# Kernel optimization log

Hardware: AMD Instinct MI355X
Metric: run time of the kernel (lower is better)

The kernel has to match this reference:

```python
import jax, jax.numpy as jnp
import numpy as np

E = 16          # num_experts
H = 2048        # hidden_size
I = 768         # moe_intermediate_size
T = 2048        # tokens (batch*seq)
K = 2           # top_k


def setup_inputs() -> dict:
    key = jax.random.key(0)
    k1, k2, k3, k4, k5 = jax.random.split(key, 5)
    hidden_states = jax.random.normal(k1, (T, H), dtype=jnp.float32)
    top_k_index = jax.random.randint(k2, (T, K), 0, E, dtype=jnp.int32)
    w = jax.random.uniform(k3, (T, K), dtype=jnp.float32)
    top_k_weights = w / jnp.sum(w, axis=-1, keepdims=True)  # softmax-like router weights
    init_std = 0.02
    gate_up_proj = jax.random.normal(k4, (E, 2 * I, H), dtype=jnp.float32) * init_std
    down_proj = jax.random.normal(k5, (E, H, I), dtype=jnp.float32) * init_std
    return {
        "hidden_states": hidden_states,
        "top_k_index": top_k_index,
        "top_k_weights": top_k_weights,
        "gate_up_proj": gate_up_proj,
        "down_proj": down_proj,
    }


def reference(hidden_states, top_k_index, top_k_weights, gate_up_proj, down_proj):
    # Combine matrix C[t, e] = sum_k top_k_weights[t, k] * 1[top_k_index[t,k] == e]
    # Tokens not routed to expert e get weight 0, so the dense-masked compute
    # below is mathematically identical to the per-expert gather/scatter loop.
    t_idx = jnp.arange(T)[:, None]
    C = jnp.zeros((T, E), dtype=hidden_states.dtype).at[t_idx, top_k_index].add(top_k_weights)

    # gate/up projection for every (token, expert): [T, E, 2I]
    gu = jnp.einsum('th,egh->teg', hidden_states, gate_up_proj)
    gate, up = jnp.split(gu, 2, axis=-1)                  # [T, E, I] each
    mid = jax.nn.silu(gate) * up                          # SwiGLU, [T, E, I]
    # down projection fused with routed combine weights -> [T, H]
    out = jnp.einsum('tei,ehi,te->th', mid, down_proj, C)
    return out
```

## Files before the change

kernel.cpp:

```cpp
#include <hip/hip_runtime.h>

#define T_TOK 2048
#define HID   2048
#define IMID  768
#define NEXP  16
#define TOPK  2

#define NPAIR (T_TOK * TOPK)
#define SLACK 64
#define NSLOT (NPAIR + SLACK)

#define BM 64
#define BK 32
#define LDSS 40

typedef __attribute__((ext_vector_type(8))) short short8;
typedef __attribute__((ext_vector_type(4))) float floatx4;

__device__ __forceinline__ short f2bf(float f) {
    union { float f; unsigned u; } v; v.f = f;
    unsigned r = (v.u + 0x7FFFu + ((v.u >> 16) & 1u)) >> 16;
    return (short)r;
}

__device__ __forceinline__ void load_cvt8(const float* __restrict__ p, short* dst) {
    float4 x = *(const float4*)p;
    float4 y = *(const float4*)(p + 4);
    short8 v;
    v[0] = f2bf(x.x); v[1] = f2bf(x.y); v[2] = f2bf(x.z); v[3] = f2bf(x.w);
    v[4] = f2bf(y.x); v[5] = f2bf(y.y); v[6] = f2bf(y.z); v[7] = f2bf(y.w);
    *(short8*)dst = v;
}

__global__ void k_count(const int* __restrict__ idx, int* __restrict__ counts) {
    int i = blockIdx.x * blockDim.x + threadIdx.x;
    if (i < NPAIR) atomicAdd(&counts[idx[i]], 1);
}

__global__ void k_scan(const int* __restrict__ counts, int* __restrict__ base,
                       int* __restrict__ cursor) {
    int s = 0;
    for (int e = 0; e < NEXP; e++) { base[e] = s; cursor[e] = s; s += counts[e]; }
}

__global__ void k_scatter(const int* __restrict__ idx, const float* __restrict__ w,
                          int* __restrict__ cursor, int* __restrict__ tok,
                          float* __restrict__ wgt) {
    int i = blockIdx.x * blockDim.x + threadIdx.x;
    if (i < NPAIR) {
        int e = idx[i];
        int p = atomicAdd(&cursor[e], 1);
        tok[p] = i / TOPK;
        wgt[p] = w[i];
    }
}

__global__ __launch_bounds__(256) void k_gemm1(
    const float* __restrict__ hs, const float* __restrict__ gup,
    const int* __restrict__ counts, const int* __restrict__ base,
    const int* __restrict__ tok, short* __restrict__ mid)
{
    const int e = blockIdx.z, rt = blockIdx.y, ct = blockIdx.x;
    const int n = counts[e];
    if (rt * BM >= n) return;
    const int rowbase = base[e] + rt * BM;

    __shared__ short sA[BM][LDSS];
    __shared__ short sBg[BM][LDSS];
    __shared__ short sBu[BM][LDSS];
    __shared__ int s_tok[BM];

    const int tid = threadIdx.x;
    if (tid < BM) s_tok[tid] = tok[rowbase + tid];
    __syncthreads();

    const int lrow = tid >> 2;
    const int cg   = (tid & 3) * 8;

    const float* aptr = hs + (size_t)s_tok[lrow] * HID + cg;
    const float* gptr = gup + (size_t)e * (2 * IMID) * HID + (size_t)(ct * 64 + lrow) * HID + cg;
    const float* uptr = gptr + (size_t)IMID * HID;

    const int wave = tid >> 6;
    const int lane = tid & 63;
    const int m16  = lane & 15;
    const int quad = lane >> 4;

    floatx4 accg[4], accu[4];
#pragma unroll
    for (int i = 0; i < 4; i++) { accg[i] = (floatx4)0.0f; accu[i] = (floatx4)0.0f; }

    for (int k0 = 0; k0 < HID; k0 += BK) {
        load_cvt8(aptr + k0, &sA[lrow][cg]);
        load_cvt8(gptr + k0, &sBg[lrow][cg]);
        load_cvt8(uptr + k0, &sBu[lrow][cg]);
        __syncthreads();
        short8 af = *(const short8*)&sA[wave * 16 + m16][quad * 8];
#pragma unroll
        for (int cf = 0; cf < 4; cf++) {
            short8 bg = *(const short8*)&sBg[cf * 16 + m16][quad * 8];
            short8 bu = *(const short8*)&sBu[cf * 16 + m16][quad * 8];
            accg[cf] = __builtin_amdgcn_mfma_f32_16x16x32_bf16(af, bg, accg[cf], 0, 0, 0);
            accu[cf] = __builtin_amdgcn_mfma_f32_16x16x32_bf16(af, bu, accu[cf], 0, 0, 0);
        }
        __syncthreads();
    }

    const int nvalid = n - rt * BM;
#pragma unroll
    for (int cf = 0; cf < 4; cf++) {
#pragma unroll
        for (int r = 0; r < 4; r++) {
            int row = wave * 16 + quad * 4 + r;
            if (row < nvalid) {
                float g = accg[cf][r], u = accu[cf][r];
                float mval = g / (1.0f + __expf(-g)) * u;
                mid[(size_t)(rowbase + row) * IMID + ct * 64 + cf * 16 + m16] = f2bf(mval);
            }
        }
    }
}

__global__ __launch_bounds__(256) void k_gemm2(
    const float* __restrict__ down, const short* __restrict__ mid,
    const int* __restrict__ counts, const int* __restrict__ base,
    const int* __restrict__ tok, const float* __restrict__ wgt,
    float* __restrict__ out)
{
    const int e = blockIdx.z, rt = blockIdx.y, ht = blockIdx.x;
    const int n = counts[e];
    if (rt * BM >= n) return;
    const int rowbase = base[e] + rt * BM;

    __shared__ short sA[BM][LDSS];
    __shared__ short sB[BM][LDSS];
    __shared__ int   s_tok[BM];
    __shared__ float s_w[BM];

    const int tid = threadIdx.x;
    if (tid < BM) { s_tok[tid] = tok[rowbase + tid]; s_w[tid] = wgt[rowbase + tid]; }

    const int lrow = tid >> 2;
    const int cg   = (tid & 3) * 8;

    const short* aptr = mid + (size_t)(rowbase + lrow) * IMID + cg;
    const float* bptr = down + (size_t)e * HID * IMID + (size_t)(ht * 64 + lrow) * IMID + cg;

    const int wave = tid >> 6;
    const int lane = tid & 63;
    const int m16  = lane & 15;
    const int quad = lane >> 4;

    floatx4 acc[4];
#pragma unroll
    for (int i = 0; i < 4; i++) acc[i] = (floatx4)0.0f;

    for (int k0 = 0; k0 < IMID; k0 += BK) {
        *(short8*)&sA[lrow][cg] = *(const short8*)(aptr + k0);
        load_cvt8(bptr + k0, &sB[lrow][cg]);
        __syncthreads();
        short8 af = *(const short8*)&sA[wave * 16 + m16][quad * 8];
#pragma unroll
        for (int cf = 0; cf < 4; cf++) {
            short8 bf_ = *(const short8*)&sB[cf * 16 + m16][quad * 8];
            acc[cf] = __builtin_amdgcn_mfma_f32_16x16x32_bf16(af, bf_, acc[cf], 0, 0, 0);
        }
        __syncthreads();
    }

    const int nvalid = n - rt * BM;
#pragma unroll
    for (int cf = 0; cf < 4; cf++) {
#pragma unroll
        for (int r = 0; r < 4; r++) {
            int row = wave * 16 + quad * 4 + r;
            if (row < nvalid) {
                int t = s_tok[row];
                float w = s_w[row];
                atomicAdd(&out[(size_t)t * HID + ht * 64 + cf * 16 + m16], w * acc[cf][r]);
            }
        }
    }
}

extern "C" void kernel_launch(void* const* d_in, const int* in_sizes, int n_in,
                              void* d_out, int out_size, void* d_ws, size_t ws_size,
                              hipStream_t stream) {
    const float* hs   = (const float*)d_in[0];
    const int*   idx  = (const int*)d_in[1];
    const float* tkw  = (const float*)d_in[2];
    const float* gup  = (const float*)d_in[3];
    const float* down = (const float*)d_in[4];
    float* out = (float*)d_out;

    char* ws = (char*)d_ws;
    int*   counts = (int*)(ws + 0);
    int*   base   = (int*)(ws + 64);
    int*   cursor = (int*)(ws + 128);
    int*   tok    = (int*)(ws + 256);
    float* wgt    = (float*)(ws + 256 + NSLOT * 4);
    short* mid    = (short*)(ws + 33792);

    hipMemsetAsync(ws, 0, 33792, stream);
    hipMemsetAsync(d_out, 0, (size_t)T_TOK * HID * sizeof(float), stream);

    k_count  <<<(NPAIR + 255) / 256, 256, 0, stream>>>(idx, counts);
    k_scan   <<<1, 1, 0, stream>>>(counts, base, cursor);
    k_scatter<<<(NPAIR + 255) / 256, 256, 0, stream>>>(idx, tkw, cursor, tok, wgt);
    k_gemm1  <<<dim3(IMID / 64, NPAIR / BM, NEXP), 256, 0, stream>>>(hs, gup, counts, base, tok, mid);
    k_gemm2  <<<dim3(HID / 64, NPAIR / BM, NEXP), 256, 0, stream>>>(down, mid, counts, base, tok, wgt, out);
}
```

Baseline: 534.5 us.

## Rewrite MoE pipeline with fused preprocessing, larger tiles, and async double-buffered loads

Routing (count, scan, scatter) now runs in one block of a single preprocessing kernel. The other blocks of that kernel pre-convert the hidden states to bf16. Both GEMMs use 128-row tiles with BK=64, a compact tile list instead of a sparse grid, and double-buffered A tiles loaded via global_load_lds with an XOR swizzle. Weight tiles are register-prefetched one step ahead. Router weights are folded into the SwiGLU output, and GEMM2 uses 128-column tiles. The aims are more data reuse, fewer launches and wasted blocks, and overlap of memory with MFMA, at the cost of higher register and LDS pressure.

```diff
diff --git a/kernel.cpp b/kernel.cpp
--- a/kernel.cpp
+++ b/kernel.cpp
@@ -1,183 +1,319 @@
 #include <hip/hip_runtime.h>
 
-#define T_TOK 2048
+#define TTOK  2048
 #define HID   2048
 #define IMID  768
 #define NEXP  16
-#define TOPK  2
-
-#define NPAIR (T_TOK * TOPK)
-#define SLACK 64
-#define NSLOT (NPAIR + SLACK)
-
-#define BM 64
-#define BK 32
-#define LDSS 40
-
-typedef __attribute__((ext_vector_type(8))) short short8;
-typedef __attribute__((ext_vector_type(4))) float floatx4;
+#define NPAIR 4096
+#define NSLOT 4224
+#define BM    128
+#define BK    64
+#define MAXT  48
+#define LDB   72
+#define ABUF  (128 * 64)
+
+typedef __attribute__((ext_vector_type(8))) short  short8;
+typedef __attribute__((ext_vector_type(4))) float  floatx4;
+typedef __attribute__((ext_vector_type(2))) unsigned uint2v;
+
+__device__ __forceinline__ unsigned pk2(float a, float b) {
+    union { float f; unsigned u; } x{a}, y{b};
+    unsigned ra = (x.u + 0x7FFFu + ((x.u >> 16) & 1u)) >> 16;
+    unsigned rb = (y.u + 0x7FFFu + ((y.u >> 16) & 1u)) & 0xFFFF0000u;
+    return ra | rb;
+}
 
 __device__ __forceinline__ short f2bf(float f) {
     union { float f; unsigned u; } v; v.f = f;
-    unsigned r = (v.u + 0x7FFFu + ((v.u >> 16) & 1u)) >> 16;
-    return (short)r;
-}
-
-__device__ __forceinline__ void load_cvt8(const float* __restrict__ p, short* dst) {
-    float4 x = *(const float4*)p;
-    float4 y = *(const float4*)(p + 4);
-    short8 v;
-    v[0] = f2bf(x.x); v[1] = f2bf(x.y); v[2] = f2bf(x.z); v[3] = f2bf(x.w);
-    v[4] = f2bf(y.x); v[5] = f2bf(y.y); v[6] = f2bf(y.z); v[7] = f2bf(y.w);
-    *(short8*)dst = v;
-}
-
-__global__ void k_count(const int* __restrict__ idx, int* __restrict__ counts) {
-    int i = blockIdx.x * blockDim.x + threadIdx.x;
-    if (i < NPAIR) atomicAdd(&counts[idx[i]], 1);
-}
-
-__global__ void k_scan(const int* __restrict__ counts, int* __restrict__ base,
-                       int* __restrict__ cursor) {
-    int s = 0;
-    for (int e = 0; e < NEXP; e++) { base[e] = s; cursor[e] = s; s += counts[e]; }
-}
-
-__global__ void k_scatter(const int* __restrict__ idx, const float* __restrict__ w,
-                          int* __restrict__ cursor, int* __restrict__ tok,
-                          float* __restrict__ wgt) {
-    int i = blockIdx.x * blockDim.x + threadIdx.x;
-    if (i < NPAIR) {
-        int e = idx[i];
-        int p = atomicAdd(&cursor[e], 1);
-        tok[p] = i / TOPK;
-        wgt[p] = w[i];
-    }
-}
-
-__global__ __launch_bounds__(256) void k_gemm1(
-    const float* __restrict__ hs, const float* __restrict__ gup,
-    const int* __restrict__ counts, const int* __restrict__ base,
-    const int* __restrict__ tok, short* __restrict__ mid)
+    return (short)((v.u + 0x7FFFu + ((v.u >> 16) & 1u)) >> 16);
+}
+
+__device__ __forceinline__ short8 cvt8(float4 a, float4 b) {
+    union { unsigned u[4]; short8 s; } r;
+    r.u[0] = pk2(a.x, a.y); r.u[1] = pk2(a.z, a.w);
+    r.u[2] = pk2(b.x, b.y); r.u[3] = pk2(b.z, b.w);
+    return r.s;
+}
+
+__device__ __forceinline__ void async_cp16(const void* g, void* l) {
+    __builtin_amdgcn_global_load_lds(
+        (const __attribute__((address_space(1))) void*)g,
+        (__attribute__((address_space(3))) void*)l, 16, 0, 0);
+}
+
+__global__ __launch_bounds__(256) void k_pre(
+    const float* __restrict__ hs, const int* __restrict__ idx,
+    const float* __restrict__ tkw, int* __restrict__ ntiles,
+    int4* __restrict__ tiles, int* __restrict__ tok,
+    float* __restrict__ wgt, short* __restrict__ X)
 {
-    const int e = blockIdx.z, rt = blockIdx.y, ct = blockIdx.x;
-    const int n = counts[e];
-    if (rt * BM >= n) return;
-    const int rowbase = base[e] + rt * BM;
-
-    __shared__ short sA[BM][LDSS];
-    __shared__ short sBg[BM][LDSS];
-    __shared__ short sBu[BM][LDSS];
-    __shared__ int s_tok[BM];
-
     const int tid = threadIdx.x;
-    if (tid < BM) s_tok[tid] = tok[rowbase + tid];
-    __syncthreads();
-
-    const int lrow = tid >> 2;
-    const int cg   = (tid & 3) * 8;
-
-    const float* aptr = hs + (size_t)s_tok[lrow] * HID + cg;
-    const float* gptr = gup + (size_t)e * (2 * IMID) * HID + (size_t)(ct * 64 + lrow) * HID + cg;
-    const float* uptr = gptr + (size_t)IMID * HID;
-
-    const int wave = tid >> 6;
-    const int lane = tid & 63;
-    const int m16  = lane & 15;
-    const int quad = lane >> 4;
-
-    floatx4 accg[4], accu[4];
-#pragma unroll
-    for (int i = 0; i < 4; i++) { accg[i] = (floatx4)0.0f; accu[i] = (floatx4)0.0f; }
-
-    for (int k0 = 0; k0 < HID; k0 += BK) {
-        load_cvt8(aptr + k0, &sA[lrow][cg]);
-        load_cvt8(gptr + k0, &sBg[lrow][cg]);
-        load_cvt8(uptr + k0, &sBu[lrow][cg]);
-        __syncthreads();
-        short8 af = *(const short8*)&sA[wave * 16 + m16][quad * 8];
-#pragma unroll
-        for (int cf = 0; cf < 4; cf++) {
-            short8 bg = *(const short8*)&sBg[cf * 16 + m16][quad * 8];
-            short8 bu = *(const short8*)&sBu[cf * 16 + m16][quad * 8];
-            accg[cf] = __builtin_amdgcn_mfma_f32_16x16x32_bf16(af, bg, accg[cf], 0, 0, 0);
-            accu[cf] = __builtin_amdgcn_mfma_f32_16x16x32_bf16(af, bu, accu[cf], 0, 0, 0);
-        }
-        __syncthreads();
-    }
-
-    const int nvalid = n - rt * BM;
-#pragma unroll
-    for (int cf = 0; cf < 4; cf++) {
-#pragma unroll
-        for (int r = 0; r < 4; r++) {
-            int row = wave * 16 + quad * 4 + r;
-            if (row < nvalid) {
-                float g = accg[cf][r], u = accu[cf][r];
-                float mval = g / (1.0f + __expf(-g)) * u;
-                mid[(size_t)(rowbase + row) * IMID + ct * 64 + cf * 16 + m16] = f2bf(mval);
-            }
-        }
-    }
-}
-
-__global__ __launch_bounds__(256) void k_gemm2(
-    const float* __restrict__ down, const short* __restrict__ mid,
-    const int* __restrict__ counts, const int* __restrict__ base,
+    if (blockIdx.x == 0) {
+        __shared__ int cnt[NEXP], cur[NEXP];
+        if (tid < NEXP) cnt[tid] = 0;
+        __syncthreads();
+        for (int i = tid; i < NPAIR; i += 256) atomicAdd(&cnt[idx[i]], 1);
+        __syncthreads();
+        if (tid == 0) {
+            int s = 0, nt = 0;
+            for (int e = 0; e < NEXP; e++) {
+                cur[e] = s;
+                int n = cnt[e];
+                for (int tt = 0; tt * BM < n; tt++) {
+                    tiles[nt] = make_int4(e, s + tt * BM, min(BM, n - tt * BM), 0);
+                    nt++;
+                }
+                s += n;
+            }
+            *ntiles = nt;
+        }
+        __syncthreads();
+        for (int i = tid; i < NPAIR; i += 256) {
+            int e = idx[i];
+            int p = atomicAdd(&cur[e], 1);
+            tok[p] = i >> 1;
+            wgt[p] = tkw[i];
+        }
+        for (int i = NPAIR + tid; i < NSLOT; i += 256) { tok[i] = 0; wgt[i] = 0.0f; }
+    } else {
+        const int row = blockIdx.x - 1;
+        const float* src = hs + (size_t)row * HID + tid * 8;
+        float4 a = *(const float4*)src;
+        float4 b = *(const float4*)(src + 4);
+        *(short8*)(X + (size_t)row * HID + tid * 8) = cvt8(a, b);
+    }
+}
+
+__global__ __launch_bounds__(256, 2) void k_gemm1(
+    const float* __restrict__ gup, const short* __restrict__ X,
+    const int* __restrict__ ntiles, const int4* __restrict__ tiles,
     const int* __restrict__ tok, const float* __restrict__ wgt,
-    float* __restrict__ out)
+    short* __restrict__ mid)
 {
-    const int e = blockIdx.z, rt = blockIdx.y, ht = blockIdx.x;
-    const int n = counts[e];
-    if (rt * BM >= n) return;
-    const int rowbase = base[e] + rt * BM;
-
-    __shared__ short sA[BM][LDSS];
-    __shared__ short sB[BM][LDSS];
+    if ((int)blockIdx.y >= *ntiles) return;
+    const int4 td = tiles[blockIdx.y];
+    const int e = td.x, rowstart = td.y, nvalid = td.z;
+    const int ct = blockIdx.x;
+
+    __shared__ short sA[2 * ABUF];
+    __shared__ short sB[128 * LDB];
     __shared__ int   s_tok[BM];
     __shared__ float s_w[BM];
 
     const int tid = threadIdx.x;
-    if (tid < BM) { s_tok[tid] = tok[rowbase + tid]; s_w[tid] = wgt[rowbase + tid]; }
-
-    const int lrow = tid >> 2;
-    const int cg   = (tid & 3) * 8;
-
-    const short* aptr = mid + (size_t)(rowbase + lrow) * IMID + cg;
-    const float* bptr = down + (size_t)e * HID * IMID + (size_t)(ht * 64 + lrow) * IMID + cg;
-
-    const int wave = tid >> 6;
-    const int lane = tid & 63;
-    const int m16  = lane & 15;
-    const int quad = lane >> 4;
-
-    floatx4 acc[4];
-#pragma unroll
-    for (int i = 0; i < 4; i++) acc[i] = (floatx4)0.0f;
-
-    for (int k0 = 0; k0 < IMID; k0 += BK) {
-        *(short8*)&sA[lrow][cg] = *(const short8*)(aptr + k0);
-        load_cvt8(bptr + k0, &sB[lrow][cg]);
-        __syncthreads();
-        short8 af = *(const short8*)&sA[wave * 16 + m16][quad * 8];
-#pragma unroll
-        for (int cf = 0; cf < 4; cf++) {
-            short8 bf_ = *(const short8*)&sB[cf * 16 + m16][quad * 8];
-            acc[cf] = __builtin_amdgcn_mfma_f32_16x16x32_bf16(af, bf_, acc[cf], 0, 0, 0);
-        }
-        __syncthreads();
-    }
-
-    const int nvalid = n - rt * BM;
-#pragma unroll
-    for (int cf = 0; cf < 4; cf++) {
+    if (tid < BM) { s_tok[tid] = tok[rowstart + tid]; s_w[tid] = wgt[rowstart + tid]; }
+    __syncthreads();
+
+    const int wave = tid >> 6, lane = tid & 63;
+    const int m16 = lane & 15, quad = lane >> 4;
+
+    const int lrow = tid >> 3;
+    const int gsw  = (tid & 7) ^ (lrow & 7);
+    const short* aga[4];
+#pragma unroll
+    for (int j = 0; j < 4; j++)
+        aga[j] = X + (size_t)s_tok[lrow + j * 32] * HID + gsw * 8;
+
+    const int colgrp = tid & 15;
+    const int rowoff = tid >> 4;
+    const float* bgate = gup + ((size_t)e * (2 * IMID) + ct * 64) * HID;
+    const float* bup   = bgate + (size_t)IMID * HID;
+
+    float4 br[8];
+    auto loadB = [&](int k0) {
+#pragma unroll
+        for (int i = 0; i < 8; i++) {
+            int brow = i * 16 + rowoff;
+            const float* p = (i < 4) ? (bgate + (size_t)brow * HID)
+                                     : (bup + (size_t)(brow - 64) * HID);
+            br[i] = *(const float4*)(p + k0 + colgrp * 4);
+        }
+    };
+    auto issueA = [&](int k0, short* dst) {
+#pragma unroll
+        for (int j = 0; j < 4; j++)
+            async_cp16(aga[j] + k0, dst + j * 2048 + wave * 512);
+    };
+
+    const int Wm = (wave >> 1) << 6;
+    const int Wi = (wave & 1) << 5;
+    floatx4 ag[4][2], au[4][2];
+#pragma unroll
+    for (int a = 0; a < 4; a++)
+#pragma unroll
+        for (int b = 0; b < 2; b++) { ag[a][b] = (floatx4)0.0f; au[a][b] = (floatx4)0.0f; }
+
+    loadB(0);
+    issueA(0, sA);
+
+    const int nsteps = HID / BK;
+    for (int ks = 0; ks < nsteps; ks++) {
+        short* Acur  = sA + (ks & 1) * ABUF;
+        short* Anext = sA + ((ks + 1) & 1) * ABUF;
+
+#pragma unroll
+        for (int i = 0; i < 8; i++) {
+            int brow = i * 16 + rowoff;
+            uint2v w2;
+            w2.x = pk2(br[i].x, br[i].y);
+            w2.y = pk2(br[i].z, br[i].w);
+            *(uint2v*)&sB[brow * LDB + colgrp * 4] = w2;
+        }
+        __syncthreads();
+
+        if (ks + 1 < nsteps) {
+            issueA((ks + 1) * BK, Anext);
+            loadB((ks + 1) * BK);
+        }
+
+#pragma unroll
+        for (int h = 0; h < 2; h++) {
+            short8 af[4];
+#pragma unroll
+            for (int mf = 0; mf < 4; mf++) {
+                int row = Wm + mf * 16 + m16;
+                int gc = (h * 4 + quad) ^ (row & 7);
+                af[mf] = *(const short8*)&Acur[row * 64 + gc * 8];
+            }
+#pragma unroll
+            for (int nf = 0; nf < 2; nf++) {
+                const short8 bg = *(const short8*)&sB[(Wi + nf * 16 + m16) * LDB + h * 32 + quad * 8];
+                const short8 bu = *(const short8*)&sB[(64 + Wi + nf * 16 + m16) * LDB + h * 32 + quad * 8];
+#pragma unroll
+                for (int mf = 0; mf < 4; mf++) {
+                    ag[mf][nf] = __builtin_amdgcn_mfma_f32_16x16x32_bf16(af[mf], bg, ag[mf][nf], 0, 0, 0);
+                    au[mf][nf] = __builtin_amdgcn_mfma_f32_16x16x32_bf16(af[mf], bu, au[mf][nf], 0, 0, 0);
+                }
+            }
+        }
+        __syncthreads();
+    }
+
+#pragma unroll
+    for (int mf = 0; mf < 4; mf++) {
 #pragma unroll
         for (int r = 0; r < 4; r++) {
-            int row = wave * 16 + quad * 4 + r;
-            if (row < nvalid) {
-                int t = s_tok[row];
-                float w = s_w[row];
-                atomicAdd(&out[(size_t)t * HID + ht * 64 + cf * 16 + m16], w * acc[cf][r]);
+            int m = Wm + mf * 16 + quad * 4 + r;
+            if (m < nvalid) {
+                float w = s_w[m];
+                size_t rowp = (size_t)(rowstart + m) * IMID + ct * 64;
+#pragma unroll
+                for (int nf = 0; nf < 2; nf++) {
+                    float g = ag[mf][nf][r], u = au[mf][nf][r];
+                    float val = g / (1.0f + __expf(-g)) * u * w;
+                    mid[rowp + Wi + nf * 16 + m16] = f2bf(val);
+                }
+            }
+        }
+    }
+}
+
+__global__ __launch_bounds__(256, 2) void k_gemm2(
+    const float* __restrict__ down, const short* __restrict__ mid,
+    const int* __restrict__ ntiles, const int4* __restrict__ tiles,
+    const int* __restrict__ tok, float* __restrict__ out)
+{
+    if ((int)blockIdx.y >= *ntiles) return;
+    const int4 td = tiles[blockIdx.y];
+    const int e = td.x, rowstart = td.y, nvalid = td.z;
+    const int ct = blockIdx.x;
+
+    __shared__ short sA[2 * ABUF];
+    __shared__ short sB[128 * LDB];
+    __shared__ int   s_tok[BM];
+
+    const int tid = threadIdx.x;
+    if (tid < BM) s_tok[tid] = tok[rowstart + tid];
+    __syncthreads();
+
+    const int wave = tid >> 6, lane = tid & 63;
+    const int m16 = lane & 15, quad = lane >> 4;
+
+    const int lrow = tid >> 3;
+    const int gsw  = (tid & 7) ^ (lrow & 7);
+    const short* aga[4];
+#pragma unroll
+    for (int j = 0; j < 4; j++)
+        aga[j] = mid + (size_t)(rowstart + lrow + j * 32) * IMID + gsw * 8;
+
+    const int colgrp = tid & 15;
+    const int rowoff = tid >> 4;
+    const float* bbase = down + ((size_t)e * HID + ct * 128) * IMID;
+
+    float4 br[8];
+    auto loadB = [&](int k0) {
+#pragma unroll
+        for (int i = 0; i < 8; i++)
+            br[i] = *(const float4*)(bbase + (size_t)(i * 16 + rowoff) * IMID + k0 + colgrp * 4);
+    };
+    auto issueA = [&](int k0, short* dst) {
+#pragma unroll
+        for (int j = 0; j < 4; j++)
+            async_cp16(aga[j] + k0, dst + j * 2048 + wave * 512);
+    };
+
+    const int Wm = (wave >> 1) << 6;
+    const int Wn = (wave & 1) << 6;
+    floatx4 acc[4][4];
+#pragma unroll
+    for (int a = 0; a < 4; a++)
+#pragma unroll
+        for (int b = 0; b < 4; b++) acc[a][b] = (floatx4)0.0f;
+
+    loadB(0);
+    issueA(0, sA);
+
+    const int nsteps = IMID / BK;
+    for (int ks = 0; ks < nsteps; ks++) {
+        short* Acur  = sA + (ks & 1) * ABUF;
+        short* Anext = sA + ((ks + 1) & 1) * ABUF;
+
+#pragma unroll
+        for (int i = 0; i < 8; i++) {
+            int brow = i * 16 + rowoff;
+            uint2v w2;
+            w2.x = pk2(br[i].x, br[i].y);
+            w2.y = pk2(br[i].z, br[i].w);
+            *(uint2v*)&sB[brow * LDB + colgrp * 4] = w2;
+        }
+        __syncthreads();
+
+        if (ks + 1 < nsteps) {
+            issueA((ks + 1) * BK, Anext);
+            loadB((ks + 1) * BK);
+        }
+
+#pragma unroll
+        for (int h = 0; h < 2; h++) {
+            short8 af[4];
+#pragma unroll
+            for (int mf = 0; mf < 4; mf++) {
+                int row = Wm + mf * 16 + m16;
+                int gc = (h * 4 + quad) ^ (row & 7);
+                af[mf] = *(const short8*)&Acur[row * 64 + gc * 8];
+            }
+#pragma unroll
+            for (int nf = 0; nf < 4; nf++) {
+                const short8 bf_ = *(const short8*)&sB[(Wn + nf * 16 + m16) * LDB + h * 32 + quad * 8];
+#pragma unroll
+                for (int mf = 0; mf < 4; mf++)
+                    acc[mf][nf] = __builtin_amdgcn_mfma_f32_16x16x32_bf16(af[mf], bf_, acc[mf][nf], 0, 0, 0);
+            }
+        }
+        __syncthreads();
+    }
+
+#pragma unroll
+    for (int mf = 0; mf < 4; mf++) {
+#pragma unroll
+        for (int r = 0; r < 4; r++) {
+            int m = Wm + mf * 16 + quad * 4 + r;
+            if (m < nvalid) {
+                int t = s_tok[m];
+                float* op = out + (size_t)t * HID + ct * 128;
+#pragma unroll
+                for (int nf = 0; nf < 4; nf++)
+                    atomicAdd(op + Wn + nf * 16 + m16, acc[mf][nf][r]);
             }
         }
     }
@@ -194,19 +330,15 @@
     float* out = (float*)d_out;
 
     char* ws = (char*)d_ws;
-    int*   counts = (int*)(ws + 0);
-    int*   base   = (int*)(ws + 64);
-    int*   cursor = (int*)(ws + 128);
-    int*   tok    = (int*)(ws + 256);
-    float* wgt    = (float*)(ws + 256 + NSLOT * 4);
-    short* mid    = (short*)(ws + 33792);
-
-    hipMemsetAsync(ws, 0, 33792, stream);
-    hipMemsetAsync(d_out, 0, (size_t)T_TOK * HID * sizeof(float), stream);
-
-    k_count  <<<(NPAIR + 255) / 256, 256, 0, stream>>>(idx, counts);
-    k_scan   <<<1, 1, 0, stream>>>(counts, base, cursor);
-    k_scatter<<<(NPAIR + 255) / 256, 256, 0, stream>>>(idx, tkw, cursor, tok, wgt);
-    k_gemm1  <<<dim3(IMID / 64, NPAIR / BM, NEXP), 256, 0, stream>>>(hs, gup, counts, base, tok, mid);
-    k_gemm2  <<<dim3(HID / 64, NPAIR / BM, NEXP), 256, 0, stream>>>(down, mid, counts, base, tok, wgt, out);
-}
+    int*   ntiles = (int*)ws;
+    int4*  tiles  = (int4*)(ws + 16);
+    int*   tok    = (int*)(ws + 1024);
+    float* wgt    = (float*)(ws + 1024 + NSLOT * 4);
+    short* mid    = (short*)(ws + 36864);
+    short* X      = (short*)(ws + 36864 + (size_t)NSLOT * IMID * 2);
+
+    hipMemsetAsync(d_out, 0, (size_t)TTOK * HID * sizeof(float), stream);
+    k_pre  <<<2049, 256, 0, stream>>>(hs, idx, tkw, ntiles, tiles, tok, wgt, X);
+    k_gemm1<<<dim3(IMID / 64, MAXT), 256, 0, stream>>>(gup, X, ntiles, tiles, tok, wgt, mid);
+    k_gemm2<<<dim3(HID / 128, MAXT), 256, 0, stream>>>(down, mid, ntiles, tiles, tok, out);
+}
```

New measurement: 443.1 us. 17.1% less time.
